# Performance work log

Hardware: AMD Instinct MI355X
Metric: run time of the kernel (lower is better)

## Reference

```python
import jax, jax.numpy as jnp
import numpy as np

B, N, D, H = 8, 1024, 768, 12
HD = D // H


def setup_inputs() -> dict:
    key = jax.random.key(0)
    ks = jax.random.split(key, 13)
    s = 0.02
    return {
        "q": jax.random.normal(ks[0], (B, N, D), jnp.float32),
        "k": jax.random.normal(ks[1], (B, N, D), jnp.float32),
        "v": jax.random.normal(ks[2], (B, N, D), jnp.float32),
        "attn_bias": jax.random.normal(ks[3], (B, H, N, N), jnp.float32),
        "attn_mask": jnp.ones((B, N, N), jnp.int32),
        "Wq": jax.random.normal(ks[4], (D, D), jnp.float32) * s,
        "bq": jnp.zeros((D,), jnp.float32),
        "Wk": jax.random.normal(ks[5], (D, D), jnp.float32) * s,
        "bk": jnp.zeros((D,), jnp.float32),
        "Wv": jax.random.normal(ks[6], (D, D), jnp.float32) * s,
        "bv": jnp.zeros((D,), jnp.float32),
        "Wo": jax.random.normal(ks[7], (D, D), jnp.float32) * s,
        "bo": jnp.zeros((D,), jnp.float32),
    }


def reference(q, k, v, attn_bias, attn_mask, Wq, bq, Wk, bk, Wv, bv, Wo, bo):
    scale = jnp.sqrt(jnp.float32(HD))
    # projections; nn.Linear computes x @ W.T + b
    qh = (q @ Wq.T + bq).reshape(B, N, H, HD).transpose(0, 2, 1, 3)  # [B,H,N,hd]
    kh = (k @ Wk.T + bk).reshape(B, N, H, HD).transpose(0, 2, 1, 3)
    vh = (v @ Wv.T + bv).reshape(B, N, H, HD).transpose(0, 2, 1, 3)
    attn = jnp.einsum("bhqd,bhkd->bhqk", qh, kh) / scale
    attn = attn + attn_bias  # Graphormer edge/spatial bias
    attn = jnp.where(attn_mask[:, None, :, :] == 0, -jnp.inf, attn)
    attn = jax.nn.softmax(attn, axis=-1)
    out = jnp.einsum("bhqk,bhkd->bhqd", attn, vh)  # [B,H,N,hd]
    out = out.transpose(0, 2, 1, 3).reshape(B, N, D)
    return out @ Wo.T + bo
```

## Files before the change

kernel.cpp:

```cpp
#include <hip/hip_runtime.h>
#include <hip/hip_bf16.h>

using f32x4  = __attribute__((ext_vector_type(4))) float;
using i32x4  = __attribute__((ext_vector_type(4))) int;
using bf16x8 = __attribute__((ext_vector_type(8))) short;
using bf16x4 = __attribute__((ext_vector_type(4))) short;

constexpr int BATCH = 8, SEQ = 1024, DIM = 768, NHEAD = 12, HDIM = 64;
constexpr int MROWS = BATCH * SEQ;

__device__ __forceinline__ short f2bf(float f) {
    union { float f; unsigned u; } x; x.f = f;
    unsigned r = (x.u + 0x7fffu + ((x.u >> 16) & 1u)) >> 16;
    return (short)r;
}
__device__ __forceinline__ float fexp2(float x) { return __builtin_amdgcn_exp2f(x); }

__device__ __forceinline__ bf16x8 cvt8(const float* p) {
    const f32x4 x0 = *(const f32x4*)p;
    const f32x4 x1 = *(const f32x4*)(p + 4);
    bf16x8 r;
    #pragma unroll
    for (int j = 0; j < 4; ++j) { r[j] = f2bf(x0[j]); r[4 + j] = f2bf(x1[j]); }
    return r;
}

__device__ __forceinline__ long kfrag_addr(int tok, int dd) {
    return ((long)(tok >> 6)) * 4096 + ((tok & 63) >> 4) * 1024 + (dd >> 5) * 512
         + ((dd >> 3) & 3) * 128 + (tok & 15) * 8 + (dd & 7);
}
__device__ __forceinline__ long vfrag_addr(int tok, int dd) {
    return ((long)(tok >> 6)) * 4096 + (dd >> 4) * 1024 + ((tok >> 5) & 1) * 512
         + ((tok >> 3) & 3) * 128 + (dd & 15) * 8 + (tok & 7);
}

__global__ __launch_bounds__(256)
void cvt_all(const float* __restrict__ q, const float* __restrict__ k,
             const float* __restrict__ v,
             const float* __restrict__ Wq, const float* __restrict__ Wk,
             const float* __restrict__ Wv, const float* __restrict__ Wo,
             short* __restrict__ qb, short* __restrict__ kb, short* __restrict__ vb,
             short* __restrict__ Wqb, short* __restrict__ Wkb,
             short* __restrict__ Wvb, short* __restrict__ Wob,
             int nbig8, int nsml8) {
    const int stride = gridDim.x * 256;
    for (int i = blockIdx.x * 256 + threadIdx.x; i < nbig8; i += stride) {
        const long base = (long)i * 8;
        *(bf16x8*)(qb + base) = cvt8(q + base);
        *(bf16x8*)(kb + base) = cvt8(k + base);
        *(bf16x8*)(vb + base) = cvt8(v + base);
    }
    for (int i = blockIdx.x * 256 + threadIdx.x; i < nsml8; i += stride) {
        const long base = (long)i * 8;
        *(bf16x8*)(Wqb + base) = cvt8(Wq + base);
        *(bf16x8*)(Wkb + base) = cvt8(Wk + base);
        *(bf16x8*)(Wvb + base) = cvt8(Wv + base);
        *(bf16x8*)(Wob + base) = cvt8(Wo + base);
    }
}

__global__ __launch_bounds__(256, 4)
void gemm_qkv(const short* __restrict__ qb, const short* __restrict__ kb,
              const short* __restrict__ vbp,
              const short* __restrict__ Wqb, const short* __restrict__ Wkb,
              const short* __restrict__ Wvb,
              const float* __restrict__ bq, const float* __restrict__ bk,
              const float* __restrict__ bv,
              short* __restrict__ Qp, short* __restrict__ Kp, short* __restrict__ Vp) {
    constexpr int K  = DIM;
    constexpr int NT = DIM / 128;
    __shared__ short As[128][72];
    __shared__ short Bs[128][72];

    const int sub = blockIdx.x % 3;
    const int bid = blockIdx.x / 3;
    const short* A = sub == 0 ? qb : sub == 1 ? kb : vbp;
    const short* W = sub == 0 ? Wqb : sub == 1 ? Wkb : Wvb;
    const float* bias = sub == 0 ? bq : sub == 1 ? bk : bv;

    const int bm = bid / NT, bn = bid % NT;
    const int m0 = bm * 128, n0 = bn * 128;
    const int t = threadIdx.x;
    const int lane = t & 63, w = t >> 6;
    const int wm = (w >> 1) * 64, wn = (w & 1) * 64;
    const int l16 = lane & 15, lg = lane >> 4;

    const int sr = t >> 1, sc = (t & 1) * 16;
    const short* aptr = A + (long)(m0 + sr) * K + sc;
    const short* wptr = W + (long)(n0 + sr) * K + sc;

    bf16x8 ra0 = *(const bf16x8*)(aptr);
    bf16x8 ra1 = *(const bf16x8*)(aptr + 8);
    bf16x8 rw0 = *(const bf16x8*)(wptr);
    bf16x8 rw1 = *(const bf16x8*)(wptr + 8);

    f32x4 acc[4][4] = {};

    for (int k0 = 0; k0 < K; k0 += 32) {
        *(bf16x8*)&As[sr][sc]     = ra0;
        *(bf16x8*)&As[sr][sc + 8] = ra1;
        *(bf16x8*)&Bs[sr][sc]     = rw0;
        *(bf16x8*)&Bs[sr][sc + 8] = rw1;
        if (k0 + 32 < K) {
            ra0 = *(const bf16x8*)(aptr + k0 + 32);
            ra1 = *(const bf16x8*)(aptr + k0 + 40);
            rw0 = *(const bf16x8*)(wptr + k0 + 32);
            rw1 = *(const bf16x8*)(wptr + k0 + 40);
        }
        __syncthreads();

        bf16x8 af[4], bfg[4];
        const int kc = lg * 8;
        #pragma unroll
        for (int mi = 0; mi < 4; ++mi)
            af[mi] = *(const bf16x8*)&As[wm + mi * 16 + l16][kc];
        #pragma unroll
        for (int ni = 0; ni < 4; ++ni)
            bfg[ni] = *(const bf16x8*)&Bs[wn + ni * 16 + l16][kc];
        #pragma unroll
        for (int mi = 0; mi < 4; ++mi)
            #pragma unroll
            for (int ni = 0; ni < 4; ++ni)
                acc[mi][ni] = __builtin_amdgcn_mfma_f32_16x16x32_bf16(
                    af[mi], bfg[ni], acc[mi][ni], 0, 0, 0);
        __syncthreads();
    }

    #pragma unroll
    for (int mi = 0; mi < 4; ++mi) {
        const int row = m0 + wm + mi * 16 + lg * 4;
        const int bb = row / SEQ;
        #pragma unroll
        for (int ni = 0; ni < 4; ++ni) {
            const int col = n0 + wn + ni * 16 + l16;
            const float bv = bias[col];
            const int hh = col >> 6, dd = col & 63;
            #pragma unroll
            for (int j = 0; j < 4; ++j) {
                float val = acc[mi][ni][j] + bv;
                if (sub == 0) {
                    Qp[(long)(row + j) * DIM + col] = f2bf(val * 0.125f);
                } else {
                    const int tok = (row % SEQ) + j;
                    const long pbase = (long)(bb * NHEAD + hh) * 65536;
                    if (sub == 1)
                        Kp[pbase + kfrag_addr(tok, dd)] = f2bf(val);
                    else
                        Vp[pbase + vfrag_addr(tok, dd)] = f2bf(val);
                }
            }
        }
    }
}

__global__ __launch_bounds__(256, 4)
void gemm_out(const short* __restrict__ A, const short* __restrict__ W,
              const float* __restrict__ bias, float* __restrict__ Cout) {
    constexpr int K  = DIM;
    constexpr int NT = DIM / 128;
    __shared__ short As[128][72];
    __shared__ short Bs[128][72];

    const int bm = blockIdx.x / NT, bn = blockIdx.x % NT;
    const int m0 = bm * 128, n0 = bn * 128;
    const int t = threadIdx.x;
    const int lane = t & 63, w = t >> 6;
    const int wm = (w >> 1) * 64, wn = (w & 1) * 64;
    const int l16 = lane & 15, lg = lane >> 4;

    const int sr = t >> 1, sc = (t & 1) * 16;
    const short* aptr = A + (long)(m0 + sr) * K + sc;
    const short* wptr = W + (long)(n0 + sr) * K + sc;

    bf16x8 ra0 = *(const bf16x8*)(aptr);
    bf16x8 ra1 = *(const bf16x8*)(aptr + 8);
    bf16x8 rw0 = *(const bf16x8*)(wptr);
    bf16x8 rw1 = *(const bf16x8*)(wptr + 8);

    f32x4 acc[4][4] = {};

    for (int k0 = 0; k0 < K; k0 += 32) {
        *(bf16x8*)&As[sr][sc]     = ra0;
        *(bf16x8*)&As[sr][sc + 8] = ra1;
        *(bf16x8*)&Bs[sr][sc]     = rw0;
        *(bf16x8*)&Bs[sr][sc + 8] = rw1;
        if (k0 + 32 < K) {
            ra0 = *(const bf16x8*)(aptr + k0 + 32);
            ra1 = *(const bf16x8*)(aptr + k0 + 40);
            rw0 = *(const bf16x8*)(wptr + k0 + 32);
            rw1 = *(const bf16x8*)(wptr + k0 + 40);
        }
        __syncthreads();

        bf16x8 af[4], bfg[4];
        const int kc = lg * 8;
        #pragma unroll
        for (int mi = 0; mi < 4; ++mi)
            af[mi] = *(const bf16x8*)&As[wm + mi * 16 + l16][kc];
        #pragma unroll
        for (int ni = 0; ni < 4; ++ni)
            bfg[ni] = *(const bf16x8*)&Bs[wn + ni * 16 + l16][kc];
        #pragma unroll
        for (int mi = 0; mi < 4; ++mi)
            #pragma unroll
            for (int ni = 0; ni < 4; ++ni)
                acc[mi][ni] = __builtin_amdgcn_mfma_f32_16x16x32_bf16(
                    af[mi], bfg[ni], acc[mi][ni], 0, 0, 0);
        __syncthreads();
    }

    #pragma unroll
    for (int mi = 0; mi < 4; ++mi) {
        const int row = m0 + wm + mi * 16 + lg * 4;
        #pragma unroll
        for (int ni = 0; ni < 4; ++ni) {
            const int col = n0 + wn + ni * 16 + l16;
            const float bv = bias[col];
            #pragma unroll
            for (int j = 0; j < 4; ++j)
                Cout[(long)(row + j) * DIM + col] = acc[mi][ni][j] + bv;
        }
    }
}

__global__ __launch_bounds__(256, 4)
void attn_kernel(const short* __restrict__ Qp, const short* __restrict__ Kt,
                 const short* __restrict__ Vt, const float* __restrict__ bias,
                 const int* __restrict__ mask, short* __restrict__ Op) {
    __shared__ float Bsm[2][64][68];

    const int d = blockIdx.x;
    const int lgc = (d & 7) * 192 + (d >> 3);
    const int qt = lgc & 15, pair = lgc >> 4;
    const int h = pair % NHEAD, b = pair / NHEAD;

    const int t = threadIdx.x, lane = t & 63, w = t >> 6;
    const int l16 = lane & 15, lg = lane >> 4;
    const int ql = w * 16 + l16;

    const int qrow = qt * 64 + ql;
    const short* qptr = Qp + (long)(b * SEQ + qrow) * DIM + h * HDIM + lg * 8;
    const bf16x8 qf0 = *(const bf16x8*)qptr;
    const bf16x8 qf1 = *(const bf16x8*)(qptr + 32);

    const short* ktile = Kt + (long)pair * 65536 + lane * 8;
    const short* vtile = Vt + (long)pair * 65536 + lane * 8;

    const int srow = t >> 4, scol = (t & 15) * 4;
    const float* bst = bias + ((long)pair * SEQ + qt * 64 + srow) * SEQ + scol;
    const int*   mst = mask + ((long)b * SEQ + qt * 64 + srow) * SEQ + scol;

    f32x4 acc_o[4] = {};
    float m_run = -1e30f, l_run = 0.f;
    constexpr float L2E = 1.4426950408889634f;

    f32x4 br[4]; i32x4 mr[4];

    auto issue_bm = [&](int kt) {
        #pragma unroll
        for (int i = 0; i < 4; ++i) {
            br[i] = __builtin_nontemporal_load((const f32x4*)(bst + (long)i * 16 * SEQ + kt * 64));
            mr[i] = *(const i32x4*)(mst + (long)i * 16 * SEQ + kt * 64);
        }
    };
    auto write_bm = [&](int buf) {
        #pragma unroll
        for (int i = 0; i < 4; ++i) {
            f32x4 o;
            #pragma unroll
            for (int j = 0; j < 4; ++j) o[j] = mr[i][j] ? br[i][j] : -1e30f;
            *(f32x4*)&Bsm[buf][i * 16 + srow][scol] = o;
        }
    };

    auto compute = [&](int kt, int buf) {
        const short* kf = ktile + kt * 4096;
        const short* vf = vtile + kt * 4096;
        short* prow = (short*)&Bsm[buf][ql][0];

        f32x4 s[4];
        __builtin_amdgcn_s_setprio(1);
        #pragma unroll
        for (int c = 0; c < 4; ++c) {
            const bf16x8 kb = *(const bf16x8*)(kf + c * 1024);
            f32x4 ci = *(const f32x4*)&Bsm[buf][ql][c * 16 + lg * 4];
            s[c] = __builtin_amdgcn_mfma_f32_16x16x32_bf16(kb, qf0, ci, 0, 0, 0);
        }
        #pragma unroll
        for (int c = 0; c < 4; ++c) {
            const bf16x8 kb = *(const bf16x8*)(kf + c * 1024 + 512);
            s[c] = __builtin_amdgcn_mfma_f32_16x16x32_bf16(kb, qf1, s[c], 0, 0, 0);
        }
        __builtin_amdgcn_s_setprio(0);

        float mt = -1e30f;
        #pragma unroll
        for (int c = 0; c < 4; ++c)
            #pragma unroll
            for (int j = 0; j < 4; ++j)
                mt = fmaxf(mt, s[c][j]);
        mt = fmaxf(mt, __shfl_xor(mt, 16));
        mt = fmaxf(mt, __shfl_xor(mt, 32));
        const float mn = fmaxf(m_run, mt);
        const float alpha = fexp2((m_run - mn) * L2E);
        m_run = mn;
        const float nm = -mn * L2E;

        float lt = 0.f;
        #pragma unroll
        for (int c = 0; c < 4; ++c) {
            bf16x4 pk;
            #pragma unroll
            for (int j = 0; j < 4; ++j) {
                const float e = fexp2(fmaf(s[c][j], L2E, nm));
                lt += e;
                pk[j] = f2bf(e);
            }
            *(bf16x4*)(prow + c * 16 + lg * 4) = pk;
        }
        lt += __shfl_xor(lt, 16);
        lt += __shfl_xor(lt, 32);
        l_run = l_run * alpha + lt;

        float al[4];
        #pragma unroll
        for (int j = 0; j < 4; ++j) al[j] = __shfl(alpha, lg * 4 + j);
        #pragma unroll
        for (int df = 0; df < 4; ++df)
            #pragma unroll
            for (int j = 0; j < 4; ++j)
                acc_o[df][j] *= al[j];

        const bf16x8 pa0 = *(const bf16x8*)(prow + lg * 8);
        const bf16x8 pa1 = *(const bf16x8*)(prow + 32 + lg * 8);
        __builtin_amdgcn_s_setprio(1);
        #pragma unroll
        for (int df = 0; df < 4; ++df) {
            const bf16x8 vb = *(const bf16x8*)(vf + df * 1024);
            acc_o[df] = __builtin_amdgcn_mfma_f32_16x16x32_bf16(pa0, vb, acc_o[df], 0, 0, 0);
        }
        #pragma unroll
        for (int df = 0; df < 4; ++df) {
            const bf16x8 vb = *(const bf16x8*)(vf + df * 1024 + 512);
            acc_o[df] = __builtin_amdgcn_mfma_f32_16x16x32_bf16(pa1, vb, acc_o[df], 0, 0, 0);
        }
        __builtin_amdgcn_s_setprio(0);
    };

    issue_bm(0);
    write_bm(0);
    issue_bm(1);
    __syncthreads();

    int cur = 0;
    for (int kt = 0; kt < 16; ++kt) {
        compute(kt, cur);
        if (kt < 15) {
            write_bm(cur ^ 1);
            if (kt < 14) issue_bm(kt + 2);
            __syncthreads();
            cur ^= 1;
        }
    }

    float linv[4];
    #pragma unroll
    for (int j = 0; j < 4; ++j)
        linv[j] = 1.f / fmaxf(__shfl(l_run, lg * 4 + j), 1e-20f);

    #pragma unroll
    for (int df = 0; df < 4; ++df) {
        #pragma unroll
        for (int j = 0; j < 4; ++j) {
            const float val = acc_o[df][j] * linv[j];
            const int row = b * SEQ + qt * 64 + w * 16 + lg * 4 + j;
            const int col = h * HDIM + df * 16 + l16;
            Op[(long)row * DIM + col] = f2bf(val);
        }
    }
}

extern "C" void kernel_launch(void* const* d_in, const int* in_sizes, int n_in,
                              void* d_out, int out_size, void* d_ws, size_t ws_size,
                              hipStream_t stream) {
    const float* q         = (const float*)d_in[0];
    const float* k         = (const float*)d_in[1];
    const float* v         = (const float*)d_in[2];
    const float* attn_bias = (const float*)d_in[3];
    const int*   attn_mask = (const int*)d_in[4];
    const float* Wq = (const float*)d_in[5];
    const float* bq = (const float*)d_in[6];
    const float* Wk = (const float*)d_in[7];
    const float* bk = (const float*)d_in[8];
    const float* Wv = (const float*)d_in[9];
    const float* bv = (const float*)d_in[10];
    const float* Wo = (const float*)d_in[11];
    const float* bo = (const float*)d_in[12];
    float* out = (float*)d_out;

    const long NED = (long)MROWS * DIM;
    const long WED = (long)DIM * DIM;
    short* Qp  = (short*)d_ws;
    short* Kp  = Qp + NED;
    short* Vp  = Kp + NED;
    short* Op  = Vp + NED;
    short* qb  = Op + NED;
    short* kb  = qb + NED;
    short* vb  = kb + NED;
    short* Wqb = vb + NED;
    short* Wkb = Wqb + WED;
    short* Wvb = Wkb + WED;
    short* Wob = Wvb + WED;

    const dim3 blk(256);

    cvt_all<<<2048, blk, 0, stream>>>(q, k, v, Wq, Wk, Wv, Wo,
                                      qb, kb, vb, Wqb, Wkb, Wvb, Wob,
                                      (int)(NED / 8), (int)(WED / 8));

    const int gemm_grid = (MROWS / 128) * (DIM / 128);
    gemm_qkv<<<3 * gemm_grid, blk, 0, stream>>>(qb, kb, vb, Wqb, Wkb, Wvb,
                                                bq, bk, bv, Qp, Kp, Vp);

    const int attn_grid = BATCH * NHEAD * (SEQ / 64);
    attn_kernel<<<attn_grid, blk, 0, stream>>>(Qp, Kp, Vp, attn_bias, attn_mask, Op);

    gemm_out<<<gemm_grid, blk, 0, stream>>>(Op, Wob, bo, out);
}
```

Measured before the change: 260.1 us.

## Fuse activation bf16 conversion into QKV GEMM and prefetch K fragments in attention

The standalone conversion pass for q/k/v activations is removed. The QKV GEMM now loads fp32 activations directly and converts them to bf16 in registers before writing shared memory, which drops a full write and re-read of three large bf16 buffers. The conversion kernel now handles only the weights. In the attention kernel, K fragments for the next tile are loaded into registers early to hide global latency, at the cost of extra registers and doubled A-operand load bytes in the GEMM.

Result: slower. 301.1 us (+15.8%).

```diff
diff --git a/kernel.cpp b/kernel.cpp
--- a/kernel.cpp
+++ b/kernel.cpp
@@ -35,22 +35,12 @@
 }
 
 __global__ __launch_bounds__(256)
-void cvt_all(const float* __restrict__ q, const float* __restrict__ k,
-             const float* __restrict__ v,
-             const float* __restrict__ Wq, const float* __restrict__ Wk,
-             const float* __restrict__ Wv, const float* __restrict__ Wo,
-             short* __restrict__ qb, short* __restrict__ kb, short* __restrict__ vb,
-             short* __restrict__ Wqb, short* __restrict__ Wkb,
-             short* __restrict__ Wvb, short* __restrict__ Wob,
-             int nbig8, int nsml8) {
+void cvt_w(const float* __restrict__ Wq, const float* __restrict__ Wk,
+           const float* __restrict__ Wv, const float* __restrict__ Wo,
+           short* __restrict__ Wqb, short* __restrict__ Wkb,
+           short* __restrict__ Wvb, short* __restrict__ Wob, int n8) {
     const int stride = gridDim.x * 256;
-    for (int i = blockIdx.x * 256 + threadIdx.x; i < nbig8; i += stride) {
-        const long base = (long)i * 8;
-        *(bf16x8*)(qb + base) = cvt8(q + base);
-        *(bf16x8*)(kb + base) = cvt8(k + base);
-        *(bf16x8*)(vb + base) = cvt8(v + base);
-    }
-    for (int i = blockIdx.x * 256 + threadIdx.x; i < nsml8; i += stride) {
+    for (int i = blockIdx.x * 256 + threadIdx.x; i < n8; i += stride) {
         const long base = (long)i * 8;
         *(bf16x8*)(Wqb + base) = cvt8(Wq + base);
         *(bf16x8*)(Wkb + base) = cvt8(Wk + base);
@@ -60,8 +50,8 @@
 }
 
 __global__ __launch_bounds__(256, 4)
-void gemm_qkv(const short* __restrict__ qb, const short* __restrict__ kb,
-              const short* __restrict__ vbp,
+void gemm_qkv(const float* __restrict__ qf, const float* __restrict__ kf,
+              const float* __restrict__ vf,
               const short* __restrict__ Wqb, const short* __restrict__ Wkb,
               const short* __restrict__ Wvb,
               const float* __restrict__ bq, const float* __restrict__ bk,
@@ -74,7 +64,7 @@
 
     const int sub = blockIdx.x % 3;
     const int bid = blockIdx.x / 3;
-    const short* A = sub == 0 ? qb : sub == 1 ? kb : vbp;
+    const float* A = sub == 0 ? qf : sub == 1 ? kf : vf;
     const short* W = sub == 0 ? Wqb : sub == 1 ? Wkb : Wvb;
     const float* bias = sub == 0 ? bq : sub == 1 ? bk : bv;
 
@@ -86,24 +76,30 @@
     const int l16 = lane & 15, lg = lane >> 4;
 
     const int sr = t >> 1, sc = (t & 1) * 16;
-    const short* aptr = A + (long)(m0 + sr) * K + sc;
+    const float* aptr = A + (long)(m0 + sr) * K + sc;
     const short* wptr = W + (long)(n0 + sr) * K + sc;
 
-    bf16x8 ra0 = *(const bf16x8*)(aptr);
-    bf16x8 ra1 = *(const bf16x8*)(aptr + 8);
+    f32x4 ra[4];
+    #pragma unroll
+    for (int i = 0; i < 4; ++i) ra[i] = *(const f32x4*)(aptr + i * 4);
     bf16x8 rw0 = *(const bf16x8*)(wptr);
     bf16x8 rw1 = *(const bf16x8*)(wptr + 8);
 
     f32x4 acc[4][4] = {};
 
     for (int k0 = 0; k0 < K; k0 += 32) {
-        *(bf16x8*)&As[sr][sc]     = ra0;
-        *(bf16x8*)&As[sr][sc + 8] = ra1;
+        short tb[16];
+        #pragma unroll
+        for (int i = 0; i < 4; ++i)
+            #pragma unroll
+            for (int j = 0; j < 4; ++j) tb[i * 4 + j] = f2bf(ra[i][j]);
+        *(bf16x8*)&As[sr][sc]     = *(bf16x8*)&tb[0];
+        *(bf16x8*)&As[sr][sc + 8] = *(bf16x8*)&tb[8];
         *(bf16x8*)&Bs[sr][sc]     = rw0;
         *(bf16x8*)&Bs[sr][sc + 8] = rw1;
         if (k0 + 32 < K) {
-            ra0 = *(const bf16x8*)(aptr + k0 + 32);
-            ra1 = *(const bf16x8*)(aptr + k0 + 40);
+            #pragma unroll
+            for (int i = 0; i < 4; ++i) ra[i] = *(const f32x4*)(aptr + k0 + 32 + i * 4);
             rw0 = *(const bf16x8*)(wptr + k0 + 32);
             rw1 = *(const bf16x8*)(wptr + k0 + 40);
         }
@@ -255,6 +251,7 @@
     constexpr float L2E = 1.4426950408889634f;
 
     f32x4 br[4]; i32x4 mr[4];
+    bf16x8 kpre[8];
 
     auto issue_bm = [&](int kt) {
         #pragma unroll
@@ -272,9 +269,16 @@
             *(f32x4*)&Bsm[buf][i * 16 + srow][scol] = o;
         }
     };
+    auto issue_k = [&](int kt) {
+        const short* kf = ktile + kt * 4096;
+        #pragma unroll
+        for (int c = 0; c < 4; ++c) {
+            kpre[c]     = *(const bf16x8*)(kf + c * 1024);
+            kpre[4 + c] = *(const bf16x8*)(kf + c * 1024 + 512);
+        }
+    };
 
     auto compute = [&](int kt, int buf) {
-        const short* kf = ktile + kt * 4096;
         const short* vf = vtile + kt * 4096;
         short* prow = (short*)&Bsm[buf][ql][0];
 
@@ -282,16 +286,15 @@
         __builtin_amdgcn_s_setprio(1);
         #pragma unroll
         for (int c = 0; c < 4; ++c) {
-            const bf16x8 kb = *(const bf16x8*)(kf + c * 1024);
             f32x4 ci = *(const f32x4*)&Bsm[buf][ql][c * 16 + lg * 4];
-            s[c] = __builtin_amdgcn_mfma_f32_16x16x32_bf16(kb, qf0, ci, 0, 0, 0);
-        }
-        #pragma unroll
-        for (int c = 0; c < 4; ++c) {
-            const bf16x8 kb = *(const bf16x8*)(kf + c * 1024 + 512);
-            s[c] = __builtin_amdgcn_mfma_f32_16x16x32_bf16(kb, qf1, s[c], 0, 0, 0);
-        }
+            s[c] = __builtin_amdgcn_mfma_f32_16x16x32_bf16(kpre[c], qf0, ci, 0, 0, 0);
+        }
+        #pragma unroll
+        for (int c = 0; c < 4; ++c)
+            s[c] = __builtin_amdgcn_mfma_f32_16x16x32_bf16(kpre[4 + c], qf1, s[c], 0, 0, 0);
         __builtin_amdgcn_s_setprio(0);
+
+        if (kt < 15) issue_k(kt + 1);
 
         float mt = -1e30f;
         #pragma unroll
@@ -350,6 +353,7 @@
     issue_bm(0);
     write_bm(0);
     issue_bm(1);
+    issue_k(0);
     __syncthreads();
 
     int cur = 0;
@@ -404,22 +408,17 @@
     short* Kp  = Qp + NED;
     short* Vp  = Kp + NED;
     short* Op  = Vp + NED;
-    short* qb  = Op + NED;
-    short* kb  = qb + NED;
-    short* vb  = kb + NED;
-    short* Wqb = vb + NED;
+    short* Wqb = Op + NED;
     short* Wkb = Wqb + WED;
     short* Wvb = Wkb + WED;
     short* Wob = Wvb + WED;
 
     const dim3 blk(256);
 
-    cvt_all<<<2048, blk, 0, stream>>>(q, k, v, Wq, Wk, Wv, Wo,
-                                      qb, kb, vb, Wqb, Wkb, Wvb, Wob,
-                                      (int)(NED / 8), (int)(WED / 8));
+    cvt_w<<<288, blk, 0, stream>>>(Wq, Wk, Wv, Wo, Wqb, Wkb, Wvb, Wob, (int)(WED / 8));
 
     const int gemm_grid = (MROWS / 128) * (DIM / 128);
-    gemm_qkv<<<3 * gemm_grid, blk, 0, stream>>>(qb, kb, vb, Wqb, Wkb, Wvb,
+    gemm_qkv<<<3 * gemm_grid, blk, 0, stream>>>(q, k, v, Wqb, Wkb, Wvb,
                                                 bq, bk, bv, Qp, Kp, Vp);
 
     const int attn_grid = BATCH * NHEAD * (SEQ / 64);
```
